# Kernel tuning notes

Measured on AMD Instinct MI355X. Metric: run time of the kernel, lower is better.

The kernel has to match this reference:

```python
import jax, jax.numpy as jnp
import numpy as np

K = 499  # kernel_size


def setup_inputs() -> dict:
    key = jax.random.key(0)
    k1, k2 = jax.random.split(key)
    B, F, T = 32, 64, 8000
    # nonnegative spectrogram input, shape (B, 1, F, T)
    x = jax.random.uniform(k1, (B, 1, F, T), dtype=jnp.float32)
    a = 0.90 + 0.099 * jax.random.uniform(k2, (F,), dtype=jnp.float32)
    w = jnp.ones((F,), dtype=jnp.float32)
    return {"x": x, "a": a, "w": w}


def _build_kernel(a, w, dtype):
    # powers[f, k] = a_f ** k, k = 0..K-2
    F = a.shape[0]
    powers = a[:, None] ** jnp.arange(K - 1, dtype=dtype)  # (F, K-1)
    C = 1.0 / powers.sum(axis=1)                            # (F,)
    neg = (-C * w)[:, None] * powers                        # (F, K-1)
    # pre-flip kernel = [1, neg_0, ..., neg_{K-2}]; flipped -> [neg_{K-2}, ..., neg_0, 1]
    kern = jnp.concatenate([neg[:, ::-1], jnp.ones((F, 1), dtype)], axis=1)  # (F, K)
    return kern[:, None, :]  # (F, 1, K) OIH, groups = F


def reference(x, a, w):
    dtype = x.dtype
    kern = _build_kernel(a.astype(dtype), w.astype(dtype), dtype)
    xs = x[:, 0]  # (B, F, T)
    # replicate (edge) pad on the left by K-1 along time
    xp = jnp.pad(xs, ((0, 0), (0, 0), (K - 1, 0)), mode="edge")
    y = jax.lax.conv_general_dilated(
        xp, kern,
        window_strides=(1,), padding="VALID",
        dimension_numbers=("NCH", "OIH", "NCH"),
        feature_group_count=xs.shape[1],
    )  # (B, F, T)
    return jnp.abs(y)[:, None]  # (B, 1, F, T)
```

## Files before the change

### kernel.cpp

```cpp
#include <hip/hip_runtime.h>
#include <math.h>


constexpr int T     = 8000;
constexpr int F     = 64;
constexpr int B     = 32;
constexpr int KM1   = 498;
constexpr int CHUNK = 512;
constexpr int CPR   = (T + CHUNK - 1) / CHUNK;

#define DPP_F(x, ctrl, rm) \
  __builtin_bit_cast(float, __builtin_amdgcn_update_dpp(0, __builtin_bit_cast(int, (x)), (ctrl), (rm), 0xf, false))

__device__ __forceinline__ double dpow(double b, int e) {
    double r = 1.0, p = b;
    while (e) { if (e & 1) r *= p; p *= p; e >>= 1; }
    return r;
}

__device__ __forceinline__ float powi(float base, int e) {
    float r = 1.0f, p = base;
    #pragma unroll
    for (int b = 0; b < 9; ++b) { r = (e & (1 << b)) ? r * p : r; p *= p; }
    return r;
}

__global__ __launch_bounds__(256) void willmore_scan_kernel(
    const float* __restrict__ x, const float* __restrict__ a,
    const float* __restrict__ w, float* __restrict__ out)
{
    const int wid   = blockIdx.x * 4 + (threadIdx.x >> 6);
    const int lane  = threadIdx.x & 63;
    const int row   = wid >> 4;
    const int chunk = wid & (CPR - 1);
    const int f     = row % F;

    const float* xr   = x   + (size_t)row * T;
    float*       orow = out + (size_t)row * T;

    const double ad     = (double)a[f];
    const double a498d  = dpow(ad, KM1);
    const double sumgeo = (1.0 - a498d) / (1.0 - ad);
    const double r_d    = dpow(ad, 8);
    const float  af     = (float)ad;
    const float  na498  = (float)(-a498d);
    const float  g      = (float)(1.0 / sumgeo) * w[f];
    const float  r1     = (float)r_d;
    const float  r2     = (float)(r_d * r_d);
    const float  r4     = (float)dpow(r_d, 4);
    const float  r8     = (float)dpow(r_d, 8);
    const float  inv_r  = (float)(1.0 / r_d);
    const float  alane  = powi(af, 8 * lane);
    const float  wA     = powi(af, 8 * ((lane & 15) + 1));
    const float  wB     = powi(af, 8 * ((lane & 31) + 1));

    const int t0   = chunk * CHUNK;
    const int tb_u = t0 + 8 * lane;
    const int tb   = min(tb_u, T - 8);

    const float4 m0 = *(const float4*)(xr + tb);
    const float4 m1 = *(const float4*)(xr + tb + 4);

    float ws8[8];
    float lv[8];
    const int lg = tb - KM1;
    if (chunk > 0) {
        const int wb = t0 - CHUNK + 8 * lane;
        const float4 w0 = *(const float4*)(xr + wb);
        const float4 w1 = *(const float4*)(xr + wb + 4);
        ws8[0]=w0.x; ws8[1]=w0.y; ws8[2]=w0.z; ws8[3]=w0.w;
        ws8[4]=w1.x; ws8[5]=w1.y; ws8[6]=w1.z; ws8[7]=w1.w;
        const float2 p0 = *(const float2*)(xr + lg);
        const float2 p1 = *(const float2*)(xr + lg + 2);
        const float2 p2 = *(const float2*)(xr + lg + 4);
        const float2 p3 = *(const float2*)(xr + lg + 6);
        lv[0]=p0.x; lv[1]=p0.y; lv[2]=p1.x; lv[3]=p1.y;
        lv[4]=p2.x; lv[5]=p2.y; lv[6]=p3.x; lv[7]=p3.y;
    } else {
        #pragma unroll
        for (int i = 0; i < 8; ++i) lv[i] = xr[max(lg + i, 0)];
    }

    float S;
    if (chunk == 0) {
        S = m0.x;
        S = xr[0] * (float)sumgeo;
    } else {
        #pragma unroll
        for (int i = 0; i < 8; ++i) { if (8 * lane + i < 14) ws8[i] = 0.0f; }
        float h = ws8[0];
        #pragma unroll
        for (int i = 1; i < 8; ++i) h = fmaf(h, af, ws8[i]);
        float contrib = powi(af, 504 - 8 * lane) * h;
        #pragma unroll
        for (int s = 1; s < 64; s <<= 1) contrib += __shfl_xor(contrib, s, 64);
        S = contrib;
    }

    const float xv[8] = {m0.x, m0.y, m0.z, m0.w, m1.x, m1.y, m1.z, m1.w};
    float u[8];
    #pragma unroll
    for (int i = 0; i < 8; ++i) u[i] = fmaf(na498, lv[i], xv[i]);

    float q = u[0];
    #pragma unroll
    for (int i = 1; i < 8; ++i) q = fmaf(q, af, u[i]);

    float G = q;
    G = fmaf(r1, DPP_F(G, 0x111, 0xf), G);
    G = fmaf(r2, DPP_F(G, 0x112, 0xf), G);
    G = fmaf(r4, DPP_F(G, 0x114, 0xf), G);
    G = fmaf(r8, DPP_F(G, 0x118, 0xf), G);
    G = fmaf(wA, DPP_F(G, 0x142, 0xa), G);
    G = fmaf(wB, DPP_F(G, 0x143, 0xc), G);

    const float E = (G - q) * inv_r;

    float s = fmaf(alane, S, E);
    float y[8];
    #pragma unroll
    for (int i = 0; i < 8; ++i) {
        y[i] = fabsf(fmaf(-g, s, xv[i]));
        s = fmaf(af, s, u[i]);
    }

    if (tb_u <= T - 8) {
        *(float4*)(orow + tb)     = make_float4(y[0], y[1], y[2], y[3]);
        *(float4*)(orow + tb + 4) = make_float4(y[4], y[5], y[6], y[7]);
    }
}

extern "C" void kernel_launch(void* const* d_in, const int* in_sizes, int n_in,
                              void* d_out, int out_size, void* d_ws, size_t ws_size,
                              hipStream_t stream) {
    const float* x = (const float*)d_in[0];
    const float* a = (const float*)d_in[1];
    const float* w = (const float*)d_in[2];
    float* out = (float*)d_out;

    const int blocks = B * F * CPR / 4;
    hipLaunchKernelGGL(willmore_scan_kernel, dim3(blocks), dim3(256), 0, stream,
                       x, a, w, out);
}
```

Baseline: 116.0 us.

## Precompute per-band constants in setup kernel, DPP window sum, nontemporal stores

Adds a one-block setup kernel that computes the per-band double-precision constants and a power table a^(8k) into workspace, so the main scan kernel loads them instead of recomputing fp64 powers in every wave. The cross-chunk window sum now uses a DPP prefix scan plus readlane instead of a shuffle-xor butterfly. Output stores become nontemporal. The cost is an extra kernel launch and dependent loads of the constants at the start of each wave.

```diff
diff --git a/kernel.cpp b/kernel.cpp
--- a/kernel.cpp
+++ b/kernel.cpp
@@ -9,6 +9,8 @@
 constexpr int CHUNK = 512;
 constexpr int CPR   = (T + CHUNK - 1) / CHUNK;
 
+typedef float nfloat4 __attribute__((ext_vector_type(4)));
+
 #define DPP_F(x, ctrl, rm) \
   __builtin_bit_cast(float, __builtin_amdgcn_update_dpp(0, __builtin_bit_cast(int, (x)), (ctrl), (rm), 0xf, false))
 
@@ -18,16 +20,35 @@
     return r;
 }
 
-__device__ __forceinline__ float powi(float base, int e) {
-    float r = 1.0f, p = base;
-    #pragma unroll
-    for (int b = 0; b < 9; ++b) { r = (e & (1 << b)) ? r * p : r; p *= p; }
-    return r;
+__global__ void willmore_setup(const float* __restrict__ a, const float* __restrict__ w,
+                               float* __restrict__ cons, float* __restrict__ tbl)
+{
+    const int tid = threadIdx.x;
+    if (tid < F) {
+        const double ad     = (double)a[tid];
+        const double a498d  = dpow(ad, KM1);
+        const double sumgeo = (1.0 - a498d) / (1.0 - ad);
+        const double r      = dpow(ad, 8);
+        float* c = cons + tid * 16;
+        c[0] = (float)ad;
+        c[1] = (float)(-a498d);
+        c[2] = (float)(1.0 / sumgeo) * w[tid];
+        c[3] = (float)r;
+        c[4] = (float)(r * r);
+        c[5] = (float)dpow(r, 4);
+        c[6] = (float)dpow(r, 8);
+        c[7] = (float)(1.0 / r);
+        c[8] = (float)sumgeo;
+    }
+    for (int i = tid; i < F * 64; i += 256) {
+        const int f = i >> 6, k = i & 63;
+        tbl[i] = (float)dpow((double)a[f], 8 * k);
+    }
 }
 
 __global__ __launch_bounds__(256) void willmore_scan_kernel(
-    const float* __restrict__ x, const float* __restrict__ a,
-    const float* __restrict__ w, float* __restrict__ out)
+    const float* __restrict__ x, const float* __restrict__ cons,
+    const float* __restrict__ tbl, float* __restrict__ out)
 {
     const int wid   = blockIdx.x * 4 + (threadIdx.x >> 6);
     const int lane  = threadIdx.x & 63;
@@ -38,21 +59,16 @@
     const float* xr   = x   + (size_t)row * T;
     float*       orow = out + (size_t)row * T;
 
-    const double ad     = (double)a[f];
-    const double a498d  = dpow(ad, KM1);
-    const double sumgeo = (1.0 - a498d) / (1.0 - ad);
-    const double r_d    = dpow(ad, 8);
-    const float  af     = (float)ad;
-    const float  na498  = (float)(-a498d);
-    const float  g      = (float)(1.0 / sumgeo) * w[f];
-    const float  r1     = (float)r_d;
-    const float  r2     = (float)(r_d * r_d);
-    const float  r4     = (float)dpow(r_d, 4);
-    const float  r8     = (float)dpow(r_d, 8);
-    const float  inv_r  = (float)(1.0 / r_d);
-    const float  alane  = powi(af, 8 * lane);
-    const float  wA     = powi(af, 8 * ((lane & 15) + 1));
-    const float  wB     = powi(af, 8 * ((lane & 31) + 1));
+    const float* c = cons + f * 16;
+    const float4 c0 = *(const float4*)(c);
+    const float4 c1 = *(const float4*)(c + 4);
+    const float  af = c0.x, na498 = c0.y, g = c0.z, r1 = c0.w;
+    const float  r2 = c1.x, r4 = c1.y, r8 = c1.z, inv_r = c1.w;
+    const float  sumgeo = c[8];
+    const float* tf = tbl + f * 64;
+    const float  alane = tf[lane];
+    const float  wA    = tf[(lane & 15) + 1];
+    const float  wB    = tf[(lane & 31) + 1];
 
     const int t0   = chunk * CHUNK;
     const int tb_u = t0 + 8 * lane;
@@ -79,22 +95,27 @@
     } else {
         #pragma unroll
         for (int i = 0; i < 8; ++i) lv[i] = xr[max(lg + i, 0)];
+        #pragma unroll
+        for (int i = 0; i < 8; ++i) ws8[i] = 0.0f;
     }
 
     float S;
-    if (chunk == 0) {
-        S = m0.x;
-        S = xr[0] * (float)sumgeo;
-    } else {
+    {
         #pragma unroll
         for (int i = 0; i < 8; ++i) { if (8 * lane + i < 14) ws8[i] = 0.0f; }
         float h = ws8[0];
         #pragma unroll
         for (int i = 1; i < 8; ++i) h = fmaf(h, af, ws8[i]);
-        float contrib = powi(af, 504 - 8 * lane) * h;
-        #pragma unroll
-        for (int s = 1; s < 64; s <<= 1) contrib += __shfl_xor(contrib, s, 64);
-        S = contrib;
+        float Gw = h;
+        Gw = fmaf(r1, DPP_F(Gw, 0x111, 0xf), Gw);
+        Gw = fmaf(r2, DPP_F(Gw, 0x112, 0xf), Gw);
+        Gw = fmaf(r4, DPP_F(Gw, 0x114, 0xf), Gw);
+        Gw = fmaf(r8, DPP_F(Gw, 0x118, 0xf), Gw);
+        Gw = fmaf(wA, DPP_F(Gw, 0x142, 0xa), Gw);
+        Gw = fmaf(wB, DPP_F(Gw, 0x143, 0xc), Gw);
+        S = __builtin_bit_cast(float,
+                __builtin_amdgcn_readlane(__builtin_bit_cast(int, Gw), 63));
+        if (chunk == 0) S = xr[0] * sumgeo;
     }
 
     const float xv[8] = {m0.x, m0.y, m0.z, m0.w, m1.x, m1.y, m1.z, m1.w};
@@ -117,16 +138,21 @@
     const float E = (G - q) * inv_r;
 
     float s = fmaf(alane, S, E);
-    float y[8];
+    nfloat4 y0, y1;
     #pragma unroll
-    for (int i = 0; i < 8; ++i) {
-        y[i] = fabsf(fmaf(-g, s, xv[i]));
+    for (int i = 0; i < 4; ++i) {
+        y0[i] = fabsf(fmaf(-g, s, xv[i]));
         s = fmaf(af, s, u[i]);
+    }
+    #pragma unroll
+    for (int i = 0; i < 4; ++i) {
+        y1[i] = fabsf(fmaf(-g, s, xv[4 + i]));
+        s = fmaf(af, s, u[4 + i]);
     }
 
     if (tb_u <= T - 8) {
-        *(float4*)(orow + tb)     = make_float4(y[0], y[1], y[2], y[3]);
-        *(float4*)(orow + tb + 4) = make_float4(y[4], y[5], y[6], y[7]);
+        __builtin_nontemporal_store(y0, (nfloat4*)(orow + tb));
+        __builtin_nontemporal_store(y1, (nfloat4*)(orow + tb + 4));
     }
 }
 
@@ -136,9 +162,12 @@
     const float* x = (const float*)d_in[0];
     const float* a = (const float*)d_in[1];
     const float* w = (const float*)d_in[2];
-    float* out = (float*)d_out;
+    float* out  = (float*)d_out;
+    float* cons = (float*)d_ws;
+    float* tbl  = cons + F * 16;
 
+    hipLaunchKernelGGL(willmore_setup, dim3(1), dim3(256), 0, stream, a, w, cons, tbl);
     const int blocks = B * F * CPR / 4;
     hipLaunchKernelGGL(willmore_scan_kernel, dim3(blocks), dim3(256), 0, stream,
-                       x, a, w, out);
+                       x, cons, tbl, out);
 }
```

Result: slower. 142.4 us (+22.8%).
